# Kernel tuning notes

Measured on AMD Instinct MI355X. Metric: run time of the kernel, lower is better.

## Reference

```python
import jax, jax.numpy as jnp
import numpy as np
import math

B, NQ, G = 512, 1, 1000
H, IN, E = 8, 256, 128
KD = E // H  # key/val dim per head = 16
C = 10.0

def setup_inputs() -> dict:
    key = jax.random.key(0)
    ks = jax.random.split(key, 10)
    inp = {
        'decoder_input': jax.random.normal(ks[0], (B, NQ, IN), jnp.float32),
        'K': jax.random.normal(ks[1], (H, B, G, KD), jnp.float32),
        'V': jax.random.normal(ks[2], (H, B, G, KD), jnp.float32),
        'V_output': jax.random.normal(ks[3], (B, G, E), jnp.float32),
        'mask': jax.random.randint(ks[4], (B, NQ, G), 0, 2, jnp.int32),
        # learned params (uniform(-stdv, stdv) init as in the torch module)
        'W_emb': jax.random.uniform(ks[5], (E, IN), jnp.float32, -1/math.sqrt(IN), 1/math.sqrt(IN)),
        'b_emb': jax.random.uniform(ks[6], (E,), jnp.float32, -1/math.sqrt(IN), 1/math.sqrt(IN)),
        'W_query': jax.random.uniform(ks[7], (H, E, KD), jnp.float32, -1/math.sqrt(KD), 1/math.sqrt(KD)),
        'W_out': jax.random.uniform(ks[8], (H, KD, E), jnp.float32, -1/math.sqrt(E), 1/math.sqrt(E)),
        'W_q': jax.random.uniform(ks[9], (1, E, E), jnp.float32, -1/math.sqrt(E), 1/math.sqrt(E)),
    }
    return inp

def reference(decoder_input, K, V, V_output, mask, W_emb, b_emb, W_query, W_out, W_q):
    # mask==0 means attention not allowed (negative adjacency after the == 0 flip)
    m = (mask == 0)[None]                                   # (1, B, NQ, G), broadcasts over heads
    emb = decoder_input @ W_emb.T + b_emb                   # (B, NQ, E)
    Q = jnp.einsum('bqi,hik->hbqk', emb, W_query)           # (H, B, NQ, KD)
    compat = jnp.einsum('hbqk,hbgk->hbqg', Q, K) / jnp.sqrt(jnp.float32(KD))
    compat = jnp.where(m, -jnp.inf, compat)
    attn = jax.nn.softmax(compat, axis=-1)
    attn = jnp.where(m, 0.0, attn)                          # zero masked entries post-softmax
    heads = jnp.einsum('hbqg,hbgk->hbqk', attn, V)          # (H, B, NQ, KD)
    context = jnp.einsum('hbqk,hke->bqe', heads, W_out)     # (B, NQ, E) multi-head out proj
    Q2 = jnp.einsum('bqe,ef->bqf', context, W_q[0])         # (B, NQ, E)
    z = jnp.einsum('bqf,bgf->bqg', Q2, V_output) / jnp.sqrt(jnp.float32(E))
    return C * jnp.tanh(z)                                  # (B, NQ, G), softmax_output=False
```

## Files before the change

kernel.cpp:

```cpp
#include <hip/hip_runtime.h>
#include <math.h>

#define GG    1000
#define HH    8
#define KDIM  16
#define EDIM  128
#define INDIM 256

__global__ __launch_bounds__(128) void k1_embq(
    const float* __restrict__ dIn,
    const float* __restrict__ Wemb,
    const float* __restrict__ bemb,
    const float* __restrict__ Wq,
    float* __restrict__ qout,
    int B)
{
    const int b = blockIdx.x, t = threadIdx.x;
    __shared__ __align__(16) float s_din[INDIM];
    __shared__ float s_emb[EDIM];

    s_din[t]       = dIn[(size_t)b * INDIM + t];
    s_din[t + 128] = dIn[(size_t)b * INDIM + t + 128];
    __syncthreads();

    float acc = bemb[t];
    const float* w = Wemb + (size_t)t * INDIM;
    #pragma unroll 4
    for (int i = 0; i < INDIM; i += 4) {
        float4 wv = *(const float4*)(w + i);
        acc += wv.x * s_din[i] + wv.y * s_din[i + 1] +
               wv.z * s_din[i + 2] + wv.w * s_din[i + 3];
    }
    s_emb[t] = acc;
    __syncthreads();

    const int h = t >> 4, k = t & 15;
    float q = 0.f;
    const float* wq = Wq + (size_t)h * EDIM * KDIM + k;
    #pragma unroll 8
    for (int e = 0; e < EDIM; ++e) q += s_emb[e] * wq[e * KDIM];
    qout[(size_t)b * EDIM + t] = q * 0.25f;
}

__global__ __launch_bounds__(256) void k2_attn(
    const float* __restrict__ K,
    const float* __restrict__ V,
    const int*   __restrict__ mask,
    const float* __restrict__ qin,
    float* __restrict__ headsout,
    int B)
{
    const int bx = blockIdx.x;
    const int b = bx % B, h = bx / B;
    const int t = threadIdx.x;

    __shared__ int   s_mask[GG];
    __shared__ float s_attn[GG];
    __shared__ __align__(16) float s_q[KDIM];
    __shared__ float s_red[8];
    __shared__ __align__(16) float s_hp[64][KDIM];
    __shared__ float s_bmax, s_binv;

    if (t < KDIM) s_q[t] = qin[(size_t)b * EDIM + h * KDIM + t];
    for (int g = t; g < GG; g += 256) s_mask[g] = mask[(size_t)b * GG + g];
    __syncthreads();

    const float* Kh = K + ((size_t)h * B + b) * (size_t)(GG * KDIM);
    float4 q0 = *(const float4*)&s_q[0];
    float4 q1 = *(const float4*)&s_q[4];
    float4 q2 = *(const float4*)&s_q[8];
    float4 q3 = *(const float4*)&s_q[12];
    float lmax = -1e30f;
    for (int g = t; g < GG; g += 256) {
        float c = -1e30f;
        if (s_mask[g] != 0) {
            const float4* kp = (const float4*)(Kh + (size_t)g * KDIM);
            float4 k0 = kp[0], k1 = kp[1], k2 = kp[2], k3 = kp[3];
            c  = q0.x * k0.x + q0.y * k0.y + q0.z * k0.z + q0.w * k0.w;
            c += q1.x * k1.x + q1.y * k1.y + q1.z * k1.z + q1.w * k1.w;
            c += q2.x * k2.x + q2.y * k2.y + q2.z * k2.z + q2.w * k2.w;
            c += q3.x * k3.x + q3.y * k3.y + q3.z * k3.z + q3.w * k3.w;
        }
        s_attn[g] = c;
        lmax = fmaxf(lmax, c);
    }
    #pragma unroll
    for (int off = 32; off; off >>= 1) lmax = fmaxf(lmax, __shfl_xor(lmax, off));
    const int wid = t >> 6;
    if ((t & 63) == 0) s_red[wid] = lmax;
    __syncthreads();
    if (t == 0) s_bmax = fmaxf(fmaxf(s_red[0], s_red[1]), fmaxf(s_red[2], s_red[3]));
    __syncthreads();
    const float m = s_bmax;

    float lsum = 0.f;
    for (int g = t; g < GG; g += 256) {
        float e = __expf(s_attn[g] - m);
        s_attn[g] = e;
        lsum += e;
    }
    #pragma unroll
    for (int off = 32; off; off >>= 1) lsum += __shfl_xor(lsum, off);
    if ((t & 63) == 0) s_red[4 + wid] = lsum;
    __syncthreads();
    if (t == 0) s_binv = 1.f / (s_red[4] + s_red[5] + s_red[6] + s_red[7]);
    __syncthreads();

    const int sub = t >> 2, k4 = t & 3;
    const float* Vh = V + ((size_t)h * B + b) * (size_t)(GG * KDIM);
    float4 acc = make_float4(0.f, 0.f, 0.f, 0.f);
    for (int g = sub; g < GG; g += 64) {
        float a = s_attn[g];
        if (a != 0.f) {
            float4 v = *(const float4*)(Vh + (size_t)g * KDIM + k4 * 4);
            acc.x += a * v.x; acc.y += a * v.y;
            acc.z += a * v.z; acc.w += a * v.w;
        }
    }
    s_hp[sub][k4 * 4 + 0] = acc.x;
    s_hp[sub][k4 * 4 + 1] = acc.y;
    s_hp[sub][k4 * 4 + 2] = acc.z;
    s_hp[sub][k4 * 4 + 3] = acc.w;
    __syncthreads();
    if (t < KDIM) {
        float s = 0.f;
        #pragma unroll
        for (int i = 0; i < 64; ++i) s += s_hp[i][t];
        headsout[(size_t)b * EDIM + h * KDIM + t] = s * s_binv;
    }
}

__global__ __launch_bounds__(256) void k3_out(
    const float* __restrict__ Vout,
    const float* __restrict__ headsin,
    const float* __restrict__ Wout,
    const float* __restrict__ WQ2,
    float* __restrict__ out,
    int B)
{
    const int bx = blockIdx.x;
    const int b = bx >> 2, chunk = bx & 3;
    const int t = threadIdx.x;
    __shared__ float s_heads[EDIM];
    __shared__ float s_ctx[EDIM];
    __shared__ __align__(16) float s_q2[EDIM];

    if (t < EDIM) s_heads[t] = headsin[(size_t)b * EDIM + t];
    __syncthreads();
    if (t < EDIM) {
        float acc = 0.f;
        #pragma unroll 8
        for (int j = 0; j < EDIM; ++j) acc += s_heads[j] * Wout[(size_t)j * EDIM + t];
        s_ctx[t] = acc;
    }
    __syncthreads();
    if (t < EDIM) {
        float acc = 0.f;
        #pragma unroll 8
        for (int e = 0; e < EDIM; ++e) acc += s_ctx[e] * WQ2[(size_t)e * EDIM + t];
        s_q2[t] = acc * 0.08838834764831845f;
    }
    __syncthreads();

    const int lane = t & 31;
    const int rowoff = t >> 5;
    float4 q = *(const float4*)&s_q2[lane * 4];
    const float* Vo = Vout + (size_t)b * (size_t)(GG * EDIM);
    const int g0 = chunk * (GG / 4);
    const int g1 = g0 + (GG / 4);
    for (int g = g0 + rowoff; g < g1; g += 8) {
        const float4* vp = (const float4*)(Vo + (size_t)g * EDIM);
        float4 v = vp[lane];
        float acc = v.x * q.x + v.y * q.y + v.z * q.z + v.w * q.w;
        #pragma unroll
        for (int off = 16; off; off >>= 1) acc += __shfl_xor(acc, off, 32);
        if (lane == 0) out[(size_t)b * GG + g] = 10.f * tanhf(acc);
    }
}

extern "C" void kernel_launch(void* const* d_in, const int* in_sizes, int n_in,
                              void* d_out, int out_size, void* d_ws, size_t ws_size,
                              hipStream_t stream) {
    const float* dIn  = (const float*)d_in[0];
    const float* K    = (const float*)d_in[1];
    const float* V    = (const float*)d_in[2];
    const float* Vout = (const float*)d_in[3];
    const int*   mask = (const int*)d_in[4];
    const float* Wemb = (const float*)d_in[5];
    const float* bemb = (const float*)d_in[6];
    const float* Wq   = (const float*)d_in[7];
    const float* Wout = (const float*)d_in[8];
    const float* WQ2  = (const float*)d_in[9];
    float* out = (float*)d_out;

    const int B = in_sizes[0] / INDIM;
    float* ws_q     = (float*)d_ws;
    float* ws_heads = ws_q + (size_t)B * EDIM;

    k1_embq<<<dim3(B), dim3(128), 0, stream>>>(dIn, Wemb, bemb, Wq, ws_q, B);
    k2_attn<<<dim3(HH * B), dim3(256), 0, stream>>>(K, V, mask, ws_q, ws_heads, B);
    k3_out<<<dim3(B * 4), dim3(256), 0, stream>>>(Vout, ws_heads, Wout, WQ2, out, B);
}
```

Before: 677.1 us.

## Split output projection into its own kernel and restructure attention loads

```diff
diff --git a/kernel.cpp b/kernel.cpp
--- a/kernel.cpp
+++ b/kernel.cpp
@@ -51,7 +51,7 @@
     int B)
 {
     const int bx = blockIdx.x;
-    const int b = bx % B, h = bx / B;
+    const int h = bx & 7, b = bx >> 3;
     const int t = threadIdx.x;
 
     __shared__ int   s_mask[GG];
@@ -70,20 +70,30 @@
     float4 q1 = *(const float4*)&s_q[4];
     float4 q2 = *(const float4*)&s_q[8];
     float4 q3 = *(const float4*)&s_q[12];
-    float lmax = -1e30f;
-    for (int g = t; g < GG; g += 256) {
-        float c = -1e30f;
-        if (s_mask[g] != 0) {
+
+    float c[4];
+    #pragma unroll
+    for (int it = 0; it < 4; ++it) {
+        const int g = t + it * 256;
+        c[it] = -1e30f;
+        if (g < GG && s_mask[g] != 0) {
             const float4* kp = (const float4*)(Kh + (size_t)g * KDIM);
             float4 k0 = kp[0], k1 = kp[1], k2 = kp[2], k3 = kp[3];
-            c  = q0.x * k0.x + q0.y * k0.y + q0.z * k0.z + q0.w * k0.w;
-            c += q1.x * k1.x + q1.y * k1.y + q1.z * k1.z + q1.w * k1.w;
-            c += q2.x * k2.x + q2.y * k2.y + q2.z * k2.z + q2.w * k2.w;
-            c += q3.x * k3.x + q3.y * k3.y + q3.z * k3.z + q3.w * k3.w;
-        }
-        s_attn[g] = c;
-        lmax = fmaxf(lmax, c);
-    }
+            float cc;
+            cc  = q0.x * k0.x + q0.y * k0.y + q0.z * k0.z + q0.w * k0.w;
+            cc += q1.x * k1.x + q1.y * k1.y + q1.z * k1.z + q1.w * k1.w;
+            cc += q2.x * k2.x + q2.y * k2.y + q2.z * k2.z + q2.w * k2.w;
+            cc += q3.x * k3.x + q3.y * k3.y + q3.z * k3.z + q3.w * k3.w;
+            c[it] = cc;
+        }
+    }
+    float lmax = -1e30f;
+    #pragma unroll
+    for (int it = 0; it < 4; ++it) {
+        const int g = t + it * 256;
+        if (g < GG) { s_attn[g] = c[it]; lmax = fmaxf(lmax, c[it]); }
+    }
+
     #pragma unroll
     for (int off = 32; off; off >>= 1) lmax = fmaxf(lmax, __shfl_xor(lmax, off));
     const int wid = t >> 6;
@@ -94,10 +104,14 @@
     const float m = s_bmax;
 
     float lsum = 0.f;
-    for (int g = t; g < GG; g += 256) {
-        float e = __expf(s_attn[g] - m);
-        s_attn[g] = e;
-        lsum += e;
+    #pragma unroll
+    for (int it = 0; it < 4; ++it) {
+        const int g = t + it * 256;
+        if (g < GG) {
+            float e = __expf(s_attn[g] - m);
+            s_attn[g] = e;
+            lsum += e;
+        }
     }
     #pragma unroll
     for (int off = 32; off; off >>= 1) lsum += __shfl_xor(lsum, off);
@@ -107,14 +121,15 @@
     __syncthreads();
 
     const int sub = t >> 2, k4 = t & 3;
-    const float* Vh = V + ((size_t)h * B + b) * (size_t)(GG * KDIM);
+    const float* Vh = V + ((size_t)h * B + b) * (size_t)(GG * KDIM) + k4 * 4;
     float4 acc = make_float4(0.f, 0.f, 0.f, 0.f);
+    #pragma unroll 4
     for (int g = sub; g < GG; g += 64) {
         float a = s_attn[g];
         if (a != 0.f) {
-            float4 v = *(const float4*)(Vh + (size_t)g * KDIM + k4 * 4);
-            acc.x += a * v.x; acc.y += a * v.y;
-            acc.z += a * v.z; acc.w += a * v.w;
+            float4 v = *(const float4*)(Vh + (size_t)g * KDIM);
+            acc.x = fmaf(a, v.x, acc.x); acc.y = fmaf(a, v.y, acc.y);
+            acc.z = fmaf(a, v.z, acc.z); acc.w = fmaf(a, v.w, acc.w);
         }
     }
     s_hp[sub][k4 * 4 + 0] = acc.x;
@@ -130,51 +145,69 @@
     }
 }
 
-__global__ __launch_bounds__(256) void k3_out(
-    const float* __restrict__ Vout,
+__global__ __launch_bounds__(128) void k25_proj(
     const float* __restrict__ headsin,
     const float* __restrict__ Wout,
     const float* __restrict__ WQ2,
-    float* __restrict__ out,
-    int B)
-{
-    const int bx = blockIdx.x;
-    const int b = bx >> 2, chunk = bx & 3;
-    const int t = threadIdx.x;
+    float* __restrict__ q2out,
+    int B)
+{
+    const int b = blockIdx.x, t = threadIdx.x;
     __shared__ float s_heads[EDIM];
     __shared__ float s_ctx[EDIM];
-    __shared__ __align__(16) float s_q2[EDIM];
-
-    if (t < EDIM) s_heads[t] = headsin[(size_t)b * EDIM + t];
-    __syncthreads();
-    if (t < EDIM) {
+
+    s_heads[t] = headsin[(size_t)b * EDIM + t];
+    __syncthreads();
+    {
         float acc = 0.f;
         #pragma unroll 8
         for (int j = 0; j < EDIM; ++j) acc += s_heads[j] * Wout[(size_t)j * EDIM + t];
         s_ctx[t] = acc;
     }
     __syncthreads();
-    if (t < EDIM) {
+    {
         float acc = 0.f;
         #pragma unroll 8
         for (int e = 0; e < EDIM; ++e) acc += s_ctx[e] * WQ2[(size_t)e * EDIM + t];
-        s_q2[t] = acc * 0.08838834764831845f;
-    }
-    __syncthreads();
-
+        q2out[(size_t)b * EDIM + t] = acc * 0.08838834764831845f;
+    }
+}
+
+__global__ __launch_bounds__(256) void k3_out(
+    const float* __restrict__ Vout,
+    const float* __restrict__ q2in,
+    float* __restrict__ out,
+    int B)
+{
+    const int bx = blockIdx.x;
+    const int b = bx >> 3, chunk = bx & 7;
+    const int t = threadIdx.x;
     const int lane = t & 31;
-    const int rowoff = t >> 5;
-    float4 q = *(const float4*)&s_q2[lane * 4];
-    const float* Vo = Vout + (size_t)b * (size_t)(GG * EDIM);
-    const int g0 = chunk * (GG / 4);
-    const int g1 = g0 + (GG / 4);
-    for (int g = g0 + rowoff; g < g1; g += 8) {
-        const float4* vp = (const float4*)(Vo + (size_t)g * EDIM);
-        float4 v = vp[lane];
-        float acc = v.x * q.x + v.y * q.y + v.z * q.z + v.w * q.w;
+    const int rowid = t >> 5;
+
+    float4 q = *(const float4*)(q2in + (size_t)b * EDIM + lane * 4);
+    const float* Vo = Vout + (size_t)b * (size_t)(GG * EDIM) + lane * 4;
+    const int g0 = chunk * (GG / 8);
+    const int g1 = g0 + (GG / 8);
+
+    for (int g = g0 + rowid; g < g1; g += 16) {
+        const int ga = g, gb = g + 8;
+        float4 va = *(const float4*)(Vo + (size_t)ga * EDIM);
+        float4 vb;
+        bool hasb = (gb < g1);
+        if (hasb) vb = *(const float4*)(Vo + (size_t)gb * EDIM);
+
+        float aa = va.x * q.x + va.y * q.y + va.z * q.z + va.w * q.w;
         #pragma unroll
-        for (int off = 16; off; off >>= 1) acc += __shfl_xor(acc, off, 32);
-        if (lane == 0) out[(size_t)b * GG + g] = 10.f * tanhf(acc);
+        for (int off = 16; off; off >>= 1) aa += __shfl_xor(aa, off, 32);
+        if (lane == 0) out[(size_t)b * GG + ga] = 10.f * tanhf(aa);
+
+        if (hasb) {
+            float ab = vb.x * q.x + vb.y * q.y + vb.z * q.z + vb.w * q.w;
+            #pragma unroll
+            for (int off = 16; off; off >>= 1) ab += __shfl_xor(ab, off, 32);
+            if (lane == 0) out[(size_t)b * GG + gb] = 10.f * tanhf(ab);
+        }
     }
 }
 
@@ -196,8 +229,10 @@
     const int B = in_sizes[0] / INDIM;
     float* ws_q     = (float*)d_ws;
     float* ws_heads = ws_q + (size_t)B * EDIM;
-
-    k1_embq<<<dim3(B), dim3(128), 0, stream>>>(dIn, Wemb, bemb, Wq, ws_q, B);
-    k2_attn<<<dim3(HH * B), dim3(256), 0, stream>>>(K, V, mask, ws_q, ws_heads, B);
-    k3_out<<<dim3(B * 4), dim3(256), 0, stream>>>(Vout, ws_heads, Wout, WQ2, out, B);
-}
+    float* ws_q2    = ws_heads + (size_t)B * EDIM;
+
+    k1_embq <<<dim3(B),      dim3(128), 0, stream>>>(dIn, Wemb, bemb, Wq, ws_q, B);
+    k2_attn <<<dim3(HH * B), dim3(256), 0, stream>>>(K, V, mask, ws_q, ws_heads, B);
+    k25_proj<<<dim3(B),      dim3(128), 0, stream>>>(ws_heads, Wout, WQ2, ws_q2, B);
+    k3_out  <<<dim3(B * 8),  dim3(256), 0, stream>>>(Vout, ws_q2, out, B);
+}
```

Result: no change. 677.7 us (+0.1%).
